# Optimization experiments

Measured on AMD Instinct MI355X. Metric: run time of the kernel, lower is better.

## Reference

```python
import jax, jax.numpy as jnp
import numpy as np

COND = 128  # mask = first 128 dims are condition (True); last 128 are transformed


def _mlp(h, W1, b1, W2, b2, W3, b3):
    h = jax.nn.relu(h @ W1 + b1)
    h = jax.nn.relu(h @ W2 + b2)
    return h @ W3 + b3


def setup_inputs() -> dict:
    key = jax.random.key(0)
    ks = jax.random.split(key, 8)
    B, D, H, T = 65536, 256, 512, 128
    s = 0.02  # small init so exp(tanh(s_vals)) is well-behaved
    inp = {
        "x": jax.random.normal(ks[0], (B, D), dtype=jnp.float32),
        "Ws1": jax.random.normal(ks[1], (COND, H), dtype=jnp.float32) * s,
        "bs1": jnp.zeros((H,), jnp.float32),
        "Ws2": jax.random.normal(ks[2], (H, H), dtype=jnp.float32) * s,
        "bs2": jnp.zeros((H,), jnp.float32),
        "Ws3": jax.random.normal(ks[3], (H, T), dtype=jnp.float32) * s,
        "bs3": jnp.zeros((T,), jnp.float32),
        "Wt1": jax.random.normal(ks[4], (COND, H), dtype=jnp.float32) * s,
        "bt1": jnp.zeros((H,), jnp.float32),
        "Wt2": jax.random.normal(ks[5], (H, H), dtype=jnp.float32) * s,
        "bt2": jnp.zeros((H,), jnp.float32),
        "Wt3": jax.random.normal(ks[6], (H, T), dtype=jnp.float32) * s,
        "bt3": jnp.zeros((T,), jnp.float32),
    }
    return inp


def reference(x, Ws1, bs1, Ws2, bs2, Ws3, bs3, Wt1, bt1, Wt2, bt2, Wt3, bt3):
    # mask gather: condition = masked dims, transform = the rest
    cond = x[:, :COND]            # [B, COND]
    x_t = x[:, COND:]             # [B, T]
    s_vals = jnp.tanh(_mlp(cond, Ws1, bs1, Ws2, bs2, Ws3, bs3))  # [B, T]
    t_vals = _mlp(cond, Wt1, bt1, Wt2, bt2, Wt3, bt3)            # [B, T]
    y_partial = x_t * jnp.exp(s_vals) + t_vals                   # forward branch (inverse=False)
    log_det = s_vals.sum(axis=1)                                 # [B]
    y = jnp.concatenate([cond, y_partial], axis=1)               # scatter back
    return (y, log_det)
```

## Files before the change

### kernel.cpp

```cpp
#include <hip/hip_runtime.h>
#include <hip/hip_bf16.h>

typedef __bf16          bf16x8_t __attribute__((ext_vector_type(8)));
typedef float           f32x4_t  __attribute__((ext_vector_type(4)));
typedef unsigned short  u16x4_t  __attribute__((ext_vector_type(4)));

#define DIN      256
#define CONDN    128
#define BM       64
#define NTHREADS 512
#define NWAVE    8

#define OFF_WS1 0
#define OFF_WS2 65536
#define OFF_WS3 327680
#define OFF_WT1 393216
#define OFF_WT2 458752
#define OFF_WT3 720896
#define W_TOTAL 786432

__global__ void prep_w(const float* __restrict__ Ws1, const float* __restrict__ Ws2,
                       const float* __restrict__ Ws3, const float* __restrict__ Wt1,
                       const float* __restrict__ Wt2, const float* __restrict__ Wt3,
                       __hip_bfloat16* __restrict__ wt) {
  int idx = blockIdx.x * blockDim.x + threadIdx.x;
  if (idx >= W_TOTAL) return;
  const float* W; int K, N, off;
  if (idx < OFF_WS2)      { W = Ws1; K = 128; N = 512; off = idx - OFF_WS1; }
  else if (idx < OFF_WS3) { W = Ws2; K = 512; N = 512; off = idx - OFF_WS2; }
  else if (idx < OFF_WT1) { W = Ws3; K = 512; N = 128; off = idx - OFF_WS3; }
  else if (idx < OFF_WT2) { W = Wt1; K = 128; N = 512; off = idx - OFF_WT1; }
  else if (idx < OFF_WT3) { W = Wt2; K = 512; N = 512; off = idx - OFF_WT2; }
  else                    { W = Wt3; K = 512; N = 128; off = idx - OFF_WT3; }
  int n = off / K;
  int k = off - n * K;
  wt[idx] = __float2bfloat16(W[k * N + n]);
}

#define SWZ(row, col) (((((col) >> 3) ^ ((row) & 7)) << 3) + ((col) & 7))

template<int KTOT, int MT, int NT>
__device__ __forceinline__ void mm_tile(const __hip_bfloat16* __restrict__ As, const int lda,
                                        const __hip_bfloat16* __restrict__ Bsrc,
                                        const int l15, const int l4, f32x4_t acc[MT][NT]) {
  const int xr = l15 & 7;
  bf16x8_t a[MT], b[NT], bn[NT];
  #pragma unroll
  for (int n = 0; n < NT; ++n)
    b[n] = *reinterpret_cast<const bf16x8_t*>(&Bsrc[(n * 16 + l15) * KTOT + l4 * 8]);
  #pragma unroll
  for (int kk = 0; kk < KTOT; kk += 32) {
    if (kk + 32 < KTOT) {
      #pragma unroll
      for (int n = 0; n < NT; ++n)
        bn[n] = *reinterpret_cast<const bf16x8_t*>(&Bsrc[(n * 16 + l15) * KTOT + kk + 32 + l4 * 8]);
    }
    #pragma unroll
    for (int m = 0; m < MT; ++m)
      a[m] = *reinterpret_cast<const bf16x8_t*>(
          &As[(m * 16 + l15) * lda + ((((kk >> 3) + l4) ^ xr) << 3)]);
    #pragma unroll
    for (int m = 0; m < MT; ++m) {
      #pragma unroll
      for (int n = 0; n < NT; ++n)
        acc[m][n] = __builtin_amdgcn_mfma_f32_16x16x32_bf16(a[m], b[n], acc[m][n], 0, 0, 0);
    }
    if (kk + 32 < KTOT) {
      #pragma unroll
      for (int n = 0; n < NT; ++n) b[n] = bn[n];
    }
  }
}

template<int MT, int NT, int LD>
__device__ __forceinline__ void relu_store(f32x4_t acc[MT][NT], const float* __restrict__ bias,
                                           const int n0, const int l15, const int l4,
                                           __hip_bfloat16* __restrict__ H) {
  #pragma unroll
  for (int n = 0; n < NT; ++n) {
    const int col = n0 + n * 16 + l15;
    const float bv = bias[col];
    #pragma unroll
    for (int m = 0; m < MT; ++m) {
      #pragma unroll
      for (int r = 0; r < 4; ++r) {
        const int row = m * 16 + l4 * 4 + r;
        float v = fmaxf(acc[m][n][r] + bv, 0.0f);
        H[row * LD + SWZ(row, col)] = __float2bfloat16(v);
      }
    }
  }
}

#define ZERO_ACC(acc, MT, NT) do {                       \
    _Pragma("unroll") for (int m_ = 0; m_ < MT; ++m_)    \
    _Pragma("unroll") for (int n_ = 0; n_ < NT; ++n_)    \
      acc[m_][n_] = (f32x4_t){0.f, 0.f, 0.f, 0.f};       \
  } while (0)

__global__ __launch_bounds__(NTHREADS, 2)
void realnvp_fused(const float* __restrict__ x, const __hip_bfloat16* __restrict__ wt,
                   const float* __restrict__ bs1, const float* __restrict__ bs2,
                   const float* __restrict__ bs3, const float* __restrict__ bt1,
                   const float* __restrict__ bt2, const float* __restrict__ bt3,
                   float* __restrict__ y, float* __restrict__ ld) {
  __shared__ __hip_bfloat16 sA[BM * CONDN];
  __shared__ __hip_bfloat16 sH[BM * 512];
  float* sLd = reinterpret_cast<float*>(sA);

  const int tid  = threadIdx.x;
  const int lane = tid & 63;
  const int wid  = tid >> 6;
  const int l15  = lane & 15;
  const int l4   = lane >> 4;
  const int row0 = blockIdx.x * BM;
  const int n0   = wid * 64;
  const int n3   = wid * 16;

  #pragma unroll
  for (int i = 0; i < 4; ++i) {
    int f = tid + i * NTHREADS;
    int r = f >> 5;
    int c = (f & 31) << 2;
    const float4 v = *reinterpret_cast<const float4*>(&x[(size_t)(row0 + r) * DIN + c]);
    *reinterpret_cast<float4*>(&y[(size_t)(row0 + r) * DIN + c]) = v;
    union { u16x4_t u; __hip_bfloat16 b[4]; } p;
    p.b[0] = __float2bfloat16(v.x); p.b[1] = __float2bfloat16(v.y);
    p.b[2] = __float2bfloat16(v.z); p.b[3] = __float2bfloat16(v.w);
    *reinterpret_cast<u16x4_t*>(&sA[r * CONDN + SWZ(r, c)]) = p.u;
  }
  __syncthreads();

  f32x4_t acc[4][4];
  f32x4_t sfrag[4], tfrag[4];

  ZERO_ACC(acc, 4, 4);
  mm_tile<128, 4, 4>(sA, CONDN, wt + OFF_WS1 + (size_t)n0 * 128, l15, l4, acc);
  relu_store<4, 4, 512>(acc, bs1, n0, l15, l4, sH);
  __syncthreads();
  ZERO_ACC(acc, 4, 4);
  mm_tile<512, 4, 4>(sH, 512, wt + OFF_WS2 + (size_t)n0 * 512, l15, l4, acc);
  __syncthreads();
  relu_store<4, 4, 512>(acc, bs2, n0, l15, l4, sH);
  __syncthreads();
  {
    f32x4_t a3[4][1];
    ZERO_ACC(a3, 4, 1);
    mm_tile<512, 4, 1>(sH, 512, wt + OFF_WS3 + (size_t)n3 * 512, l15, l4, a3);
    #pragma unroll
    for (int m = 0; m < 4; ++m) sfrag[m] = a3[m][0];
  }
  __syncthreads();

  ZERO_ACC(acc, 4, 4);
  mm_tile<128, 4, 4>(sA, CONDN, wt + OFF_WT1 + (size_t)n0 * 128, l15, l4, acc);
  relu_store<4, 4, 512>(acc, bt1, n0, l15, l4, sH);
  __syncthreads();
  ZERO_ACC(acc, 4, 4);
  mm_tile<512, 4, 4>(sH, 512, wt + OFF_WT2 + (size_t)n0 * 512, l15, l4, acc);
  __syncthreads();
  relu_store<4, 4, 512>(acc, bt2, n0, l15, l4, sH);
  __syncthreads();
  {
    f32x4_t a3[4][1];
    ZERO_ACC(a3, 4, 1);
    mm_tile<512, 4, 1>(sH, 512, wt + OFF_WT3 + (size_t)n3 * 512, l15, l4, a3);
    #pragma unroll
    for (int m = 0; m < 4; ++m) tfrag[m] = a3[m][0];
  }

  const float bsv = bs3[n3 + l15];
  const float btv = bt3[n3 + l15];
  #pragma unroll
  for (int m = 0; m < 4; ++m) {
    #pragma unroll
    for (int r = 0; r < 4; ++r) {
      const int rl   = m * 16 + l4 * 4 + r;
      const int grow = row0 + rl;
      const int col  = n3 + l15;
      float s = tanhf(sfrag[m][r] + bsv);
      float t = tfrag[m][r] + btv;
      float xv = x[(size_t)grow * DIN + CONDN + col];
      y[(size_t)grow * DIN + CONDN + col] = xv * expf(s) + t;
      float ss = s;
      ss += __shfl_xor(ss, 1);
      ss += __shfl_xor(ss, 2);
      ss += __shfl_xor(ss, 4);
      ss += __shfl_xor(ss, 8);
      if (l15 == 0) sLd[wid * BM + rl] = ss;
    }
  }
  __syncthreads();
  if (tid < BM) {
    float v = 0.f;
    #pragma unroll
    for (int w = 0; w < NWAVE; ++w) v += sLd[w * BM + tid];
    ld[row0 + tid] = v;
  }
}

extern "C" void kernel_launch(void* const* d_in, const int* in_sizes, int n_in,
                              void* d_out, int out_size, void* d_ws, size_t ws_size,
                              hipStream_t stream) {
  const float* x   = (const float*)d_in[0];
  const float* Ws1 = (const float*)d_in[1];
  const float* bs1 = (const float*)d_in[2];
  const float* Ws2 = (const float*)d_in[3];
  const float* bs2 = (const float*)d_in[4];
  const float* Ws3 = (const float*)d_in[5];
  const float* bs3 = (const float*)d_in[6];
  const float* Wt1 = (const float*)d_in[7];
  const float* bt1 = (const float*)d_in[8];
  const float* Wt2 = (const float*)d_in[9];
  const float* bt2 = (const float*)d_in[10];
  const float* Wt3 = (const float*)d_in[11];
  const float* bt3 = (const float*)d_in[12];

  const int Btot = in_sizes[0] / DIN;
  float* y  = (float*)d_out;
  float* ld = (float*)d_out + (size_t)Btot * DIN;
  __hip_bfloat16* wt = (__hip_bfloat16*)d_ws;

  prep_w<<<(W_TOTAL + 255) / 256, 256, 0, stream>>>(Ws1, Ws2, Ws3, Wt1, Wt2, Wt3, wt);
  realnvp_fused<<<Btot / BM, NTHREADS, 0, stream>>>(x, wt, bs1, bs2, bs3,
                                                    bt1, bt2, bt3, y, ld);
}
```

Measured before the change: 240.4 us.

## Halve block to 4 waves with wider per-wave N tiles and global A loads

Cuts the block from 8 to 4 waves, so each wave computes 128 hidden columns (4x8 MFMA tiles) instead of 64, which doubles the reuse of each A fragment. The first-layer GEMMs now read x straight from global memory and convert to bf16 in registers, removing the sA staging buffer and its barrier. The B prefetch double-buffering is replaced by a plain loop unrolled by two. In exchange, per-thread register pressure rises sharply (128 accumulator floats), which may cause spills or lower occupancy, and layer 1 now reads x twice from global memory.

```diff
diff --git a/kernel.cpp b/kernel.cpp
--- a/kernel.cpp
+++ b/kernel.cpp
@@ -3,13 +3,12 @@
 
 typedef __bf16          bf16x8_t __attribute__((ext_vector_type(8)));
 typedef float           f32x4_t  __attribute__((ext_vector_type(4)));
-typedef unsigned short  u16x4_t  __attribute__((ext_vector_type(4)));
 
 #define DIN      256
 #define CONDN    128
 #define BM       64
-#define NTHREADS 512
-#define NWAVE    8
+#define NTHREADS 256
+#define NWAVE    4
 
 #define OFF_WS1 0
 #define OFF_WS2 65536
@@ -39,41 +38,65 @@
 
 #define SWZ(row, col) (((((col) >> 3) ^ ((row) & 7)) << 3) + ((col) & 7))
 
-template<int KTOT, int MT, int NT>
-__device__ __forceinline__ void mm_tile(const __hip_bfloat16* __restrict__ As, const int lda,
+template<int KTOT, int MTT, int NT>
+__device__ __forceinline__ void mm_ldsA(const __hip_bfloat16* __restrict__ As,
                                         const __hip_bfloat16* __restrict__ Bsrc,
-                                        const int l15, const int l4, f32x4_t acc[MT][NT]) {
+                                        const int l15, const int l4, f32x4_t acc[MTT][NT]) {
   const int xr = l15 & 7;
-  bf16x8_t a[MT], b[NT], bn[NT];
-  #pragma unroll
-  for (int n = 0; n < NT; ++n)
-    b[n] = *reinterpret_cast<const bf16x8_t*>(&Bsrc[(n * 16 + l15) * KTOT + l4 * 8]);
-  #pragma unroll
-  for (int kk = 0; kk < KTOT; kk += 32) {
-    if (kk + 32 < KTOT) {
-      #pragma unroll
-      for (int n = 0; n < NT; ++n)
-        bn[n] = *reinterpret_cast<const bf16x8_t*>(&Bsrc[(n * 16 + l15) * KTOT + kk + 32 + l4 * 8]);
-    }
-    #pragma unroll
-    for (int m = 0; m < MT; ++m)
+  const __hip_bfloat16* bp = Bsrc + (size_t)l15 * KTOT + l4 * 8;
+  #pragma unroll 2
+  for (int s = 0; s < KTOT / 32; ++s) {
+    bf16x8_t b[NT], a[MTT];
+    #pragma unroll
+    for (int n = 0; n < NT; ++n)
+      b[n] = *reinterpret_cast<const bf16x8_t*>(bp + (size_t)n * 16 * KTOT + s * 32);
+    #pragma unroll
+    for (int m = 0; m < MTT; ++m)
       a[m] = *reinterpret_cast<const bf16x8_t*>(
-          &As[(m * 16 + l15) * lda + ((((kk >> 3) + l4) ^ xr) << 3)]);
-    #pragma unroll
-    for (int m = 0; m < MT; ++m) {
+          &As[(m * 16 + l15) * 512 + (((s * 4 + l4) ^ xr) << 3)]);
+    #pragma unroll
+    for (int m = 0; m < MTT; ++m) {
       #pragma unroll
       for (int n = 0; n < NT; ++n)
         acc[m][n] = __builtin_amdgcn_mfma_f32_16x16x32_bf16(a[m], b[n], acc[m][n], 0, 0, 0);
     }
-    if (kk + 32 < KTOT) {
+  }
+}
+
+template<int NT>
+__device__ __forceinline__ void mm_gA(const float* __restrict__ xbase,
+                                      const __hip_bfloat16* __restrict__ Bsrc,
+                                      const int l15, const int l4, f32x4_t acc[4][NT]) {
+  const __hip_bfloat16* bp = Bsrc + (size_t)l15 * 128 + l4 * 8;
+  #pragma unroll
+  for (int s = 0; s < 4; ++s) {
+    bf16x8_t b[NT], a[4];
+    #pragma unroll
+    for (int n = 0; n < NT; ++n)
+      b[n] = *reinterpret_cast<const bf16x8_t*>(bp + (size_t)n * 16 * 128 + s * 32);
+    #pragma unroll
+    for (int m = 0; m < 4; ++m) {
+      const float* xp = xbase + (size_t)(m * 16 + l15) * DIN + s * 32 + l4 * 8;
+      const float4 v0 = *reinterpret_cast<const float4*>(xp);
+      const float4 v1 = *reinterpret_cast<const float4*>(xp + 4);
+      union { bf16x8_t v; __hip_bfloat16 b8[8]; } av;
+      av.b8[0] = __float2bfloat16(v0.x); av.b8[1] = __float2bfloat16(v0.y);
+      av.b8[2] = __float2bfloat16(v0.z); av.b8[3] = __float2bfloat16(v0.w);
+      av.b8[4] = __float2bfloat16(v1.x); av.b8[5] = __float2bfloat16(v1.y);
+      av.b8[6] = __float2bfloat16(v1.z); av.b8[7] = __float2bfloat16(v1.w);
+      a[m] = av.v;
+    }
+    #pragma unroll
+    for (int m = 0; m < 4; ++m) {
       #pragma unroll
-      for (int n = 0; n < NT; ++n) b[n] = bn[n];
-    }
-  }
-}
-
-template<int MT, int NT, int LD>
-__device__ __forceinline__ void relu_store(f32x4_t acc[MT][NT], const float* __restrict__ bias,
+      for (int n = 0; n < NT; ++n)
+        acc[m][n] = __builtin_amdgcn_mfma_f32_16x16x32_bf16(a[m], b[n], acc[m][n], 0, 0, 0);
+    }
+  }
+}
+
+template<int MTT, int NT>
+__device__ __forceinline__ void relu_store(f32x4_t acc[MTT][NT], const float* __restrict__ bias,
                                            const int n0, const int l15, const int l4,
                                            __hip_bfloat16* __restrict__ H) {
   #pragma unroll
@@ -81,21 +104,21 @@
     const int col = n0 + n * 16 + l15;
     const float bv = bias[col];
     #pragma unroll
-    for (int m = 0; m < MT; ++m) {
+    for (int m = 0; m < MTT; ++m) {
       #pragma unroll
       for (int r = 0; r < 4; ++r) {
         const int row = m * 16 + l4 * 4 + r;
         float v = fmaxf(acc[m][n][r] + bv, 0.0f);
-        H[row * LD + SWZ(row, col)] = __float2bfloat16(v);
+        H[row * 512 + SWZ(row, col)] = __float2bfloat16(v);
       }
     }
   }
 }
 
-#define ZERO_ACC(acc, MT, NT) do {                       \
-    _Pragma("unroll") for (int m_ = 0; m_ < MT; ++m_)    \
-    _Pragma("unroll") for (int n_ = 0; n_ < NT; ++n_)    \
-      acc[m_][n_] = (f32x4_t){0.f, 0.f, 0.f, 0.f};       \
+#define ZERO_ACC(acc, MTT, NT) do {                       \
+    _Pragma("unroll") for (int m_ = 0; m_ < MTT; ++m_)    \
+    _Pragma("unroll") for (int n_ = 0; n_ < NT; ++n_)     \
+      acc[m_][n_] = (f32x4_t){0.f, 0.f, 0.f, 0.f};        \
   } while (0)
 
 __global__ __launch_bounds__(NTHREADS, 2)
@@ -104,9 +127,8 @@
                    const float* __restrict__ bs3, const float* __restrict__ bt1,
                    const float* __restrict__ bt2, const float* __restrict__ bt3,
                    float* __restrict__ y, float* __restrict__ ld) {
-  __shared__ __hip_bfloat16 sA[BM * CONDN];
   __shared__ __hip_bfloat16 sH[BM * 512];
-  float* sLd = reinterpret_cast<float*>(sA);
+  float* sLd = reinterpret_cast<float*>(sH);
 
   const int tid  = threadIdx.x;
   const int lane = tid & 63;
@@ -114,75 +136,79 @@
   const int l15  = lane & 15;
   const int l4   = lane >> 4;
   const int row0 = blockIdx.x * BM;
-  const int n0   = wid * 64;
-  const int n3   = wid * 16;
-
-  #pragma unroll
-  for (int i = 0; i < 4; ++i) {
+  const int n0   = wid * 128;
+  const int n3   = wid * 32;
+  const float* xbase = x + (size_t)row0 * DIN;
+
+  #pragma unroll
+  for (int i = 0; i < 8; ++i) {
     int f = tid + i * NTHREADS;
     int r = f >> 5;
     int c = (f & 31) << 2;
-    const float4 v = *reinterpret_cast<const float4*>(&x[(size_t)(row0 + r) * DIN + c]);
+    const float4 v = *reinterpret_cast<const float4*>(&xbase[(size_t)r * DIN + c]);
     *reinterpret_cast<float4*>(&y[(size_t)(row0 + r) * DIN + c]) = v;
-    union { u16x4_t u; __hip_bfloat16 b[4]; } p;
-    p.b[0] = __float2bfloat16(v.x); p.b[1] = __float2bfloat16(v.y);
-    p.b[2] = __float2bfloat16(v.z); p.b[3] = __float2bfloat16(v.w);
-    *reinterpret_cast<u16x4_t*>(&sA[r * CONDN + SWZ(r, c)]) = p.u;
-  }
-  __syncthreads();
-
-  f32x4_t acc[4][4];
-  f32x4_t sfrag[4], tfrag[4];
-
-  ZERO_ACC(acc, 4, 4);
-  mm_tile<128, 4, 4>(sA, CONDN, wt + OFF_WS1 + (size_t)n0 * 128, l15, l4, acc);
-  relu_store<4, 4, 512>(acc, bs1, n0, l15, l4, sH);
-  __syncthreads();
-  ZERO_ACC(acc, 4, 4);
-  mm_tile<512, 4, 4>(sH, 512, wt + OFF_WS2 + (size_t)n0 * 512, l15, l4, acc);
-  __syncthreads();
-  relu_store<4, 4, 512>(acc, bs2, n0, l15, l4, sH);
+  }
+
+  f32x4_t acc[4][8];
+  f32x4_t sfrag[4][2], tfrag[4][2];
+
+  ZERO_ACC(acc, 4, 8);
+  mm_gA<8>(xbase, wt + OFF_WS1 + (size_t)n0 * 128, l15, l4, acc);
+  relu_store<4, 8>(acc, bs1, n0, l15, l4, sH);
+  __syncthreads();
+  ZERO_ACC(acc, 4, 8);
+  mm_ldsA<512, 4, 8>(sH, wt + OFF_WS2 + (size_t)n0 * 512, l15, l4, acc);
+  __syncthreads();
+  relu_store<4, 8>(acc, bs2, n0, l15, l4, sH);
   __syncthreads();
   {
-    f32x4_t a3[4][1];
-    ZERO_ACC(a3, 4, 1);
-    mm_tile<512, 4, 1>(sH, 512, wt + OFF_WS3 + (size_t)n3 * 512, l15, l4, a3);
-    #pragma unroll
-    for (int m = 0; m < 4; ++m) sfrag[m] = a3[m][0];
-  }
-  __syncthreads();
-
-  ZERO_ACC(acc, 4, 4);
-  mm_tile<128, 4, 4>(sA, CONDN, wt + OFF_WT1 + (size_t)n0 * 128, l15, l4, acc);
-  relu_store<4, 4, 512>(acc, bt1, n0, l15, l4, sH);
-  __syncthreads();
-  ZERO_ACC(acc, 4, 4);
-  mm_tile<512, 4, 4>(sH, 512, wt + OFF_WT2 + (size_t)n0 * 512, l15, l4, acc);
-  __syncthreads();
-  relu_store<4, 4, 512>(acc, bt2, n0, l15, l4, sH);
+    f32x4_t a3[4][2];
+    ZERO_ACC(a3, 4, 2);
+    mm_ldsA<512, 4, 2>(sH, wt + OFF_WS3 + (size_t)n3 * 512, l15, l4, a3);
+    #pragma unroll
+    for (int m = 0; m < 4; ++m) { sfrag[m][0] = a3[m][0]; sfrag[m][1] = a3[m][1]; }
+  }
+
+  ZERO_ACC(acc, 4, 8);
+  mm_gA<8>(xbase, wt + OFF_WT1 + (size_t)n0 * 128, l15, l4, acc);
+  __syncthreads();
+  relu_store<4, 8>(acc, bt1, n0, l15, l4, sH);
+  __syncthreads();
+  ZERO_ACC(acc, 4, 8);
+  mm_ldsA<512, 4, 8>(sH, wt + OFF_WT2 + (size_t)n0 * 512, l15, l4, acc);
+  __syncthreads();
+  relu_store<4, 8>(acc, bt2, n0, l15, l4, sH);
   __syncthreads();
   {
-    f32x4_t a3[4][1];
-    ZERO_ACC(a3, 4, 1);
-    mm_tile<512, 4, 1>(sH, 512, wt + OFF_WT3 + (size_t)n3 * 512, l15, l4, a3);
-    #pragma unroll
-    for (int m = 0; m < 4; ++m) tfrag[m] = a3[m][0];
-  }
-
-  const float bsv = bs3[n3 + l15];
-  const float btv = bt3[n3 + l15];
+    f32x4_t a3[4][2];
+    ZERO_ACC(a3, 4, 2);
+    mm_ldsA<512, 4, 2>(sH, wt + OFF_WT3 + (size_t)n3 * 512, l15, l4, a3);
+    #pragma unroll
+    for (int m = 0; m < 4; ++m) { tfrag[m][0] = a3[m][0]; tfrag[m][1] = a3[m][1]; }
+  }
+  __syncthreads();
+
+  const float bs0 = bs3[n3 + l15];
+  const float bs1v = bs3[n3 + 16 + l15];
+  const float bt0 = bt3[n3 + l15];
+  const float bt1v = bt3[n3 + 16 + l15];
   #pragma unroll
   for (int m = 0; m < 4; ++m) {
     #pragma unroll
     for (int r = 0; r < 4; ++r) {
       const int rl   = m * 16 + l4 * 4 + r;
       const int grow = row0 + rl;
-      const int col  = n3 + l15;
-      float s = tanhf(sfrag[m][r] + bsv);
-      float t = tfrag[m][r] + btv;
-      float xv = x[(size_t)grow * DIN + CONDN + col];
-      y[(size_t)grow * DIN + CONDN + col] = xv * expf(s) + t;
-      float ss = s;
+      const int c0   = n3 + l15;
+      const int c1   = n3 + 16 + l15;
+      float s0 = tanhf(sfrag[m][0][r] + bs0);
+      float s1 = tanhf(sfrag[m][1][r] + bs1v);
+      float t0 = tfrag[m][0][r] + bt0;
+      float t1 = tfrag[m][1][r] + bt1v;
+      float xv0 = x[(size_t)grow * DIN + CONDN + c0];
+      float xv1 = x[(size_t)grow * DIN + CONDN + c1];
+      y[(size_t)grow * DIN + CONDN + c0] = xv0 * expf(s0) + t0;
+      y[(size_t)grow * DIN + CONDN + c1] = xv1 * expf(s1) + t1;
+      float ss = s0 + s1;
       ss += __shfl_xor(ss, 1);
       ss += __shfl_xor(ss, 2);
       ss += __shfl_xor(ss, 4);
```

Result: slower. 341.7 us (+42.1%).
